# Optimization experiments

Measured on AMD Instinct MI355X. Metric: run time of the kernel, lower is better.

## Reference

```python
import jax, jax.numpy as jnp
import numpy as np

# RRFU config (matches init_kwargs)
S = 2          # scale_factor
G = 4          # groups
K = 3          # sample_k
C = 64         # in_channels
B, H, W_IN = 4, 128, 128
SC = S * S     # s_c
KC = K * K     # sample_c (3x3 = 9)


def setup_inputs() -> dict:
    key = jax.random.key(0)
    ks = jax.random.split(key, 9)
    x = jax.random.normal(ks[0], (B, C, H, W_IN), jnp.float32)
    # 1x1 conv weights stored as (out_ch, in_ch); std chosen per module's init
    # (mask convs are zero-init in the original; use small random so math is nontrivial)
    w_off = jax.random.normal(ks[1], (G * SC * 2, C), jnp.float32) * 0.001
    b_off = jnp.zeros((G * SC * 2,), jnp.float32)
    w_offm = jax.random.normal(ks[2], (G * SC * 2, C), jnp.float32) * 0.01
    b_offm = jnp.zeros((G * SC * 2,), jnp.float32)
    w_sk = jax.random.normal(ks[3], (KC, C), jnp.float32) * 0.005
    b_sk = jnp.zeros((KC,), jnp.float32)
    w_km = jax.random.normal(ks[4], (KC, C), jnp.float32) * 0.01
    b_km = jnp.zeros((KC,), jnp.float32)
    return {"x": x, "w_off": w_off, "b_off": b_off, "w_offm": w_offm,
            "b_offm": b_offm, "w_sk": w_sk, "b_sk": b_sk, "w_km": w_km, "b_km": b_km}


def _conv1x1(x, w, b):
    return jnp.einsum('oc,bchw->bohw', w, x) + b[None, :, None, None]


def _bilinear_border(img, iy, ix):
    """img: (Cg,H,W); iy,ix: (Ho,Wo) pixel coords. grid_sample bilinear, padding_mode='border'."""
    Hh, Ww = img.shape[1], img.shape[2]
    ix = jnp.clip(ix, 0.0, Ww - 1.0)
    iy = jnp.clip(iy, 0.0, Hh - 1.0)
    x0 = jnp.floor(ix)
    y0 = jnp.floor(iy)
    wx = ix - x0
    wy = iy - y0
    x0i = x0.astype(jnp.int32)
    y0i = y0.astype(jnp.int32)
    x1i = jnp.minimum(x0i + 1, Ww - 1)
    y1i = jnp.minimum(y0i + 1, Hh - 1)
    v00 = img[:, y0i, x0i]
    v01 = img[:, y0i, x1i]
    v10 = img[:, y1i, x0i]
    v11 = img[:, y1i, x1i]
    return (v00 * (1 - wx) * (1 - wy) + v01 * wx * (1 - wy)
            + v10 * (1 - wx) * wy + v11 * wx * wy)


def reference(x, w_off, b_off, w_offm, b_offm, w_sk, b_sk, w_km, b_km):
    b0, c0, h0, w0 = x.shape
    # learned offsets, gated by sigmoid mask
    off = _conv1x1(x, w_off, b_off) * jax.nn.sigmoid(_conv1x1(x, w_offm, b_offm))
    bg = b0 * G
    # (b, g*S*S*2, h, w) -> (bg, S, S, 2, h, w) -> (bg, h, S, w, S, 2) -> (bg, S*h, S*w, 2)
    off = off.reshape(bg, S, S, 2, h0, w0).transpose(0, 4, 1, 5, 2, 3).reshape(bg, S * h0, S * w0, 2)
    Ho, Wo = S * h0, S * w0
    # coord_base + offset, normalized then un-normalized for align_corners=False grid_sample
    cx = jnp.arange(Wo, dtype=x.dtype) + 0.5
    cy = jnp.arange(Ho, dtype=x.dtype) + 0.5
    ix = (cx[None, None, :] + off[..., 0]) * (w0 / Wo) - 0.5  # (bg, Ho, Wo)
    iy = (cy[None, :, None] + off[..., 1]) * (h0 / Ho) - 0.5
    x_r = x.reshape(bg, c0 // G, h0, w0)
    x_def = jax.vmap(_bilinear_border)(x_r, iy, ix).reshape(b0, c0, Ho, Wo)
    # CARAFE-style dynamic reassembly: softmax kernel over 3x3 neighborhood
    sk = _conv1x1(x_def, w_sk, b_sk) * jax.nn.sigmoid(_conv1x1(x_def, w_km, b_km))
    skn = jax.nn.softmax(sk, axis=1)  # (b, 9, Ho, Wo)
    pad = K // 2
    xp = jnp.pad(x_def, ((0, 0), (0, 0), (pad, pad), (pad, pad)))  # zero pad like F.unfold
    out = jnp.zeros_like(x_def)
    for ky in range(K):  # fixed 3x3 taps; avoids materializing (b,c,9,Ho,Wo)
        for kx in range(K):
            out = out + skn[:, ky * K + kx][:, None] * xp[:, :, ky:ky + Ho, kx:kx + Wo]
    return out
```

## Files before the change

### kernel.cpp

```cpp
#include <hip/hip_runtime.h>
#include <hip/hip_fp16.h>

constexpr int Bc  = 4;
constexpr int Cc  = 64;
constexpr int H0  = 128;
constexpr int W0  = 128;
constexpr int HW  = H0 * W0;
constexpr int Gc  = 4;
constexpr int CG  = Cc / Gc;
constexpr int HOc = H0 * 2;
constexpr int WOc = W0 * 2;

constexpr int TW = 16;
constexpr int TH = 8;
constexpr int HX = TW + 2;
constexpr int HY = TH + 2;
constexpr int NHALO = HX * HY;
constexpr int NTASK = Gc * NHALO;

constexpr int SXC = 10;
constexpr int SYC = 6;
constexpr int SN  = SXC * SYC;

__global__ __launch_bounds__(256) void k0_offsets(
    const float* __restrict__ x,
    const float* __restrict__ w_off,  const float* __restrict__ b_off,
    const float* __restrict__ w_offm, const float* __restrict__ b_offm,
    float* __restrict__ offbuf)
{
    const int bg = blockIdx.y;
    const int b  = bg >> 2, g = bg & 3;
    const int pp = blockIdx.x * 256 + threadIdx.x;
    const int h  = pp >> 6;
    const int w  = (pp & 63) << 1;

    const float2* xp = reinterpret_cast<const float2*>(
        x + (size_t)b * Cc * HW + h * W0 + w);
    const float* Wa = w_off  + (g * 8) * Cc;
    const float* Wm = w_offm + (g * 8) * Cc;

    float a0[8], a1[8], m0[8], m1[8];
#pragma unroll
    for (int r = 0; r < 8; ++r) { a0[r] = a1[r] = m0[r] = m1[r] = 0.f; }

#pragma unroll 4
    for (int c = 0; c < Cc; ++c) {
        const float2 xv = xp[c * (HW >> 1)];
#pragma unroll
        for (int r = 0; r < 8; ++r) {
            const float wa = Wa[r * Cc + c];
            const float wm = Wm[r * Cc + c];
            a0[r] = fmaf(wa, xv.x, a0[r]);
            a1[r] = fmaf(wa, xv.y, a1[r]);
            m0[r] = fmaf(wm, xv.x, m0[r]);
            m1[r] = fmaf(wm, xv.y, m1[r]);
        }
    }

    float* ob = offbuf + ((size_t)bg * 8) * HW + h * W0 + w;
#pragma unroll
    for (int r = 0; r < 8; ++r) {
        const float ba = b_off [g * 8 + r];
        const float bm = b_offm[g * 8 + r];
        const float o0 = (a0[r] + ba) / (1.f + __expf(-(m0[r] + bm)));
        const float o1 = (a1[r] + ba) / (1.f + __expf(-(m1[r] + bm)));
        *reinterpret_cast<float2*>(&ob[(size_t)r * HW]) = make_float2(o0, o1);
    }
}

__global__ __launch_bounds__(256) void k1_fused(
    const float* __restrict__ x, const float* __restrict__ offbuf,
    const float* __restrict__ w_sk, const float* __restrict__ b_sk,
    const float* __restrict__ w_km, const float* __restrict__ b_km,
    float* __restrict__ out)
{
    __shared__ __half xd[Cc][NHALO];
    __shared__ float  ovl[Cc * SN];
    float* xstage = ovl;
    float* kmb    = ovl;
    float* sknb   = ovl + 128 * 9;

    const int b    = blockIdx.y;
    const int tile = blockIdx.x;
    const int ox = (tile & 15) * TW;
    const int oy = (tile >> 4) * TH;
    const int t  = threadIdx.x;
    const int syr = (oy >> 1) - 1;
    const int sxr = (ox >> 1) - 1;

    const float* xb = x + (size_t)b * Cc * HW;

    for (int i = t; i < Cc * SN; i += 256) {
        const int c   = i / SN;
        const int rem = i - c * SN;
        const int r   = rem / SXC;
        const int j   = rem - r * SXC;
        const int yy  = min(max(syr + r, 0), H0 - 1);
        const int xx  = min(max(sxr + j, 0), W0 - 1);
        xstage[i] = xb[(size_t)c * HW + yy * W0 + xx];
    }
    __syncthreads();

    for (int task = t; task < NTASK; task += 256) {
        const int g   = task / NHALO;
        const int pix = task - g * NHALO;
        const int hy  = pix / HX;
        const int hx  = pix - hy * HX;
        const int gy  = oy - 1 + hy;
        const int gx  = ox - 1 + hx;
        if (gy < 0 || gy >= HOc || gx < 0 || gx >= WOc) {
#pragma unroll 4
            for (int c = 0; c < CG; ++c) xd[g * CG + c][pix] = __half(0.f);
            continue;
        }
        const int sy = gy & 1, sx = gx & 1;
        const int h  = gy >> 1, w  = gx >> 1;
        const int r0 = sy * 4 + sx * 2;
        const int bg = b * 4 + g;
        const size_t obase = ((size_t)bg * 8 + r0) * HW + h * W0 + w;
        const float offx = offbuf[obase];
        const float offy = offbuf[obase + HW];

        float ix = ((float)gx + 0.5f + offx) * 0.5f - 0.5f;
        float iy = ((float)gy + 0.5f + offy) * 0.5f - 0.5f;
        ix = fminf(fmaxf(ix, 0.f), (float)(W0 - 1));
        iy = fminf(fmaxf(iy, 0.f), (float)(H0 - 1));
        const float x0f = floorf(ix), y0f = floorf(iy);
        const float wx = ix - x0f,   wy = iy - y0f;
        const int x0 = (int)x0f, y0 = (int)y0f;
        const int x1 = min(x0 + 1, W0 - 1), y1 = min(y0 + 1, H0 - 1);
        const float w00 = (1.f - wx) * (1.f - wy);
        const float w01 = wx * (1.f - wy);
        const float w10 = (1.f - wx) * wy;
        const float w11 = wx * wy;

        const int j0 = x0 - sxr, j1 = x1 - sxr;
        const int i0 = y0 - syr, i1 = y1 - syr;
        const bool inl = (j0 >= 0) & (j1 < SXC) & (i0 >= 0) & (i1 < SYC);

        if (inl) {
            const int o00 = i0 * SXC + j0, o01 = i0 * SXC + j1;
            const int o10 = i1 * SXC + j0, o11 = i1 * SXC + j1;
            const float* s = xstage + (g * CG) * SN;
#pragma unroll 4
            for (int c = 0; c < CG; ++c) {
                const float* pc = s + c * SN;
                const float v = w00 * pc[o00] + w01 * pc[o01]
                              + w10 * pc[o10] + w11 * pc[o11];
                xd[g * CG + c][pix] = __float2half(v);
            }
        } else {
            const int o00 = y0 * W0 + x0, o01 = y0 * W0 + x1;
            const int o10 = y1 * W0 + x0, o11 = y1 * W0 + x1;
            const float* xg = xb + (size_t)(g * CG) * HW;
#pragma unroll 4
            for (int c = 0; c < CG; ++c) {
                const float* pc = xg + (size_t)c * HW;
                const float v = w00 * pc[o00] + w01 * pc[o01]
                              + w10 * pc[o10] + w11 * pc[o11];
                xd[g * CG + c][pix] = __float2half(v);
            }
        }
    }
    __syncthreads();

    {
        const int p   = t & 127;
        const int ctr = ((p >> 4) + 1) * HX + (p & 15) + 1;
        float acc[9];
#pragma unroll
        for (int k = 0; k < 9; ++k) acc[k] = 0.f;

        if (t < 128) {
            for (int c = 0; c < Cc; ++c) {
                const float xv = __half2float(xd[c][ctr]);
#pragma unroll
                for (int k = 0; k < 9; ++k)
                    acc[k] = fmaf(w_sk[k * Cc + c], xv, acc[k]);
            }
        } else {
            for (int c = 0; c < Cc; ++c) {
                const float xv = __half2float(xd[c][ctr]);
#pragma unroll
                for (int k = 0; k < 9; ++k)
                    acc[k] = fmaf(w_km[k * Cc + c], xv, acc[k]);
            }
#pragma unroll
            for (int k = 0; k < 9; ++k) kmb[p * 9 + k] = acc[k];
        }
        __syncthreads();

        if (t < 128) {
            float sv[9], mx = -1e30f;
#pragma unroll
            for (int k = 0; k < 9; ++k) {
                const float z = kmb[p * 9 + k] + b_km[k];
                sv[k] = (acc[k] + b_sk[k]) / (1.f + __expf(-z));
                mx = fmaxf(mx, sv[k]);
            }
            float sum = 0.f;
#pragma unroll
            for (int k = 0; k < 9; ++k) { sv[k] = __expf(sv[k] - mx); sum += sv[k]; }
            const float inv = 1.f / sum;
#pragma unroll
            for (int k = 0; k < 9; ++k) sknb[p * 9 + k] = sv[k] * inv;
        }
    }
    __syncthreads();

    {
        const int sq    = t & 31;
        const int chunk = t >> 5;
        const int sqx = sq & 7, sqy = sq >> 3;
        const int hx0 = 2 * sqx, hy0 = 2 * sqy;
        const int p00 = (2 * sqy) * TW + 2 * sqx;

        float s00[9], s01[9], s10[9], s11[9];
#pragma unroll
        for (int k = 0; k < 9; ++k) {
            s00[k] = sknb[p00 * 9 + k];        s01[k] = sknb[(p00 + 1) * 9 + k];
            s10[k] = sknb[(p00 + TW) * 9 + k]; s11[k] = sknb[(p00 + TW + 1) * 9 + k];
        }
        const int orow0 = oy + 2 * sqy, ocol0 = ox + 2 * sqx;

#pragma unroll 2
        for (int i = 0; i < 8; ++i) {
            const int c = chunk * 8 + i;
            const __half* xc = &xd[c][0];
            float wd[4][4];
#pragma unroll
            for (int ry = 0; ry < 4; ++ry) {
                const int base = (hy0 + ry) * HX + hx0;
                const __half2 u0 = *reinterpret_cast<const __half2*>(&xc[base]);
                const __half2 u1 = *reinterpret_cast<const __half2*>(&xc[base + 2]);
                const float2 f0 = __half22float2(u0);
                const float2 f1 = __half22float2(u1);
                wd[ry][0] = f0.x; wd[ry][1] = f0.y; wd[ry][2] = f1.x; wd[ry][3] = f1.y;
            }
            float a00 = 0.f, a01 = 0.f, a10 = 0.f, a11 = 0.f;
#pragma unroll
            for (int ky = 0; ky < 3; ++ky)
#pragma unroll
                for (int kx = 0; kx < 3; ++kx) {
                    const int k = ky * 3 + kx;
                    a00 = fmaf(s00[k], wd[ky    ][kx    ], a00);
                    a01 = fmaf(s01[k], wd[ky    ][kx + 1], a01);
                    a10 = fmaf(s10[k], wd[ky + 1][kx    ], a10);
                    a11 = fmaf(s11[k], wd[ky + 1][kx + 1], a11);
                }
            float* ob = out + ((size_t)(b * Cc + c)) * (HOc * WOc)
                            + (size_t)orow0 * WOc + ocol0;
            *reinterpret_cast<float2*>(ob)       = make_float2(a00, a01);
            *reinterpret_cast<float2*>(ob + WOc) = make_float2(a10, a11);
        }
    }
}

extern "C" void kernel_launch(void* const* d_in, const int* in_sizes, int n_in,
                              void* d_out, int out_size, void* d_ws, size_t ws_size,
                              hipStream_t stream)
{
    const float* x      = (const float*)d_in[0];
    const float* w_off  = (const float*)d_in[1];
    const float* b_off  = (const float*)d_in[2];
    const float* w_offm = (const float*)d_in[3];
    const float* b_offm = (const float*)d_in[4];
    const float* w_sk   = (const float*)d_in[5];
    const float* b_sk   = (const float*)d_in[6];
    const float* w_km   = (const float*)d_in[7];
    const float* b_km   = (const float*)d_in[8];
    float* outp = (float*)d_out;

    const size_t off_bytes = (size_t)Bc * Gc * 8 * HW * sizeof(float);
    if (ws_size < off_bytes) return;
    float* offbuf = (float*)d_ws;

    dim3 blk(256);
    dim3 g0(HW / (2 * 256), Bc * Gc);
    hipLaunchKernelGGL(k0_offsets, g0, blk, 0, stream,
                       x, w_off, b_off, w_offm, b_offm, offbuf);

    dim3 g1(512, Bc);
    hipLaunchKernelGGL(k1_fused, g1, blk, 0, stream,
                       x, offbuf, w_sk, b_sk, w_km, b_km, outp);
}
```

Measured before the change: 68.31 us.

## Fuse offset conv into main kernel and stage input via direct global-to-LDS loads

Removes the separate offset kernel and its global offset buffer. Each block now computes the gated offset 1x1 conv for its 10x6 source patch from the staged input in shared memory, and reads offsets from LDS. The input staging uses global_load_lds, the launch becomes a 1D grid with a swizzled block-to-tile mapping, and launch bounds request 3 blocks per CU. This trades a kernel launch and the offset-buffer round trip for redundant offset compute on halo pixels, extra LDS, and a serial 64-channel loop per block in which only 60 of 64 lanes per wave are active.

Result: slower. 151.0 us (+121.1%).

```diff
diff --git a/kernel.cpp b/kernel.cpp
--- a/kernel.cpp
+++ b/kernel.cpp
@@ -21,67 +21,36 @@
 constexpr int SXC = 10;
 constexpr int SYC = 6;
 constexpr int SN  = SXC * SYC;
-
-__global__ __launch_bounds__(256) void k0_offsets(
+constexpr int NROW = Gc * 8;
+
+constexpr int NTILE = (HOc / TH) * (WOc / TW);
+constexpr int NB    = NTILE * Bc;
+
+__device__ __forceinline__ void gl_lds4(const float* g, float* l) {
+    __builtin_amdgcn_global_load_lds(
+        (const __attribute__((address_space(1))) void*)g,
+        (__attribute__((address_space(3)))       void*)l, 4, 0, 0);
+}
+
+__global__ __launch_bounds__(256, 3) void k1_fused(
     const float* __restrict__ x,
     const float* __restrict__ w_off,  const float* __restrict__ b_off,
     const float* __restrict__ w_offm, const float* __restrict__ b_offm,
-    float* __restrict__ offbuf)
-{
-    const int bg = blockIdx.y;
-    const int b  = bg >> 2, g = bg & 3;
-    const int pp = blockIdx.x * 256 + threadIdx.x;
-    const int h  = pp >> 6;
-    const int w  = (pp & 63) << 1;
-
-    const float2* xp = reinterpret_cast<const float2*>(
-        x + (size_t)b * Cc * HW + h * W0 + w);
-    const float* Wa = w_off  + (g * 8) * Cc;
-    const float* Wm = w_offm + (g * 8) * Cc;
-
-    float a0[8], a1[8], m0[8], m1[8];
-#pragma unroll
-    for (int r = 0; r < 8; ++r) { a0[r] = a1[r] = m0[r] = m1[r] = 0.f; }
-
-#pragma unroll 4
-    for (int c = 0; c < Cc; ++c) {
-        const float2 xv = xp[c * (HW >> 1)];
-#pragma unroll
-        for (int r = 0; r < 8; ++r) {
-            const float wa = Wa[r * Cc + c];
-            const float wm = Wm[r * Cc + c];
-            a0[r] = fmaf(wa, xv.x, a0[r]);
-            a1[r] = fmaf(wa, xv.y, a1[r]);
-            m0[r] = fmaf(wm, xv.x, m0[r]);
-            m1[r] = fmaf(wm, xv.y, m1[r]);
-        }
-    }
-
-    float* ob = offbuf + ((size_t)bg * 8) * HW + h * W0 + w;
-#pragma unroll
-    for (int r = 0; r < 8; ++r) {
-        const float ba = b_off [g * 8 + r];
-        const float bm = b_offm[g * 8 + r];
-        const float o0 = (a0[r] + ba) / (1.f + __expf(-(m0[r] + bm)));
-        const float o1 = (a1[r] + ba) / (1.f + __expf(-(m1[r] + bm)));
-        *reinterpret_cast<float2*>(&ob[(size_t)r * HW]) = make_float2(o0, o1);
-    }
-}
-
-__global__ __launch_bounds__(256) void k1_fused(
-    const float* __restrict__ x, const float* __restrict__ offbuf,
-    const float* __restrict__ w_sk, const float* __restrict__ b_sk,
-    const float* __restrict__ w_km, const float* __restrict__ b_km,
+    const float* __restrict__ w_sk,   const float* __restrict__ b_sk,
+    const float* __restrict__ w_km,   const float* __restrict__ b_km,
     float* __restrict__ out)
 {
     __shared__ __half xd[Cc][NHALO];
+    __shared__ float  offs[NROW][SN];
     __shared__ float  ovl[Cc * SN];
     float* xstage = ovl;
     float* kmb    = ovl;
     float* sknb   = ovl + 128 * 9;
 
-    const int b    = blockIdx.y;
-    const int tile = blockIdx.x;
+    const int bid  = blockIdx.x;
+    const int sw   = (bid & 7) * (NB / 8) + (bid >> 3);
+    const int b    = sw >> 9;
+    const int tile = sw & 511;
     const int ox = (tile & 15) * TW;
     const int oy = (tile >> 4) * TH;
     const int t  = threadIdx.x;
@@ -97,7 +66,32 @@
         const int j   = rem - r * SXC;
         const int yy  = min(max(syr + r, 0), H0 - 1);
         const int xx  = min(max(sxr + j, 0), W0 - 1);
-        xstage[i] = xb[(size_t)c * HW + yy * W0 + xx];
+        gl_lds4(xb + (size_t)c * HW + yy * W0 + xx, &xstage[i]);
+    }
+    __syncthreads();
+
+    {
+        const int wave = t >> 6, lane = t & 63;
+        if (lane < SN) {
+            const int R0 = wave * 8;
+            float a[8], m[8];
+#pragma unroll
+            for (int q = 0; q < 8; ++q) { a[q] = 0.f; m[q] = 0.f; }
+            for (int c = 0; c < Cc; ++c) {
+                const float xv = xstage[c * SN + lane];
+#pragma unroll
+                for (int q = 0; q < 8; ++q) {
+                    a[q] = fmaf(w_off [(R0 + q) * Cc + c], xv, a[q]);
+                    m[q] = fmaf(w_offm[(R0 + q) * Cc + c], xv, m[q]);
+                }
+            }
+#pragma unroll
+            for (int q = 0; q < 8; ++q) {
+                const float av = a[q] + b_off [R0 + q];
+                const float mv = m[q] + b_offm[R0 + q];
+                offs[R0 + q][lane] = av / (1.f + __expf(-mv));
+            }
+        }
     }
     __syncthreads();
 
@@ -116,10 +110,9 @@
         const int sy = gy & 1, sx = gx & 1;
         const int h  = gy >> 1, w  = gx >> 1;
         const int r0 = sy * 4 + sx * 2;
-        const int bg = b * 4 + g;
-        const size_t obase = ((size_t)bg * 8 + r0) * HW + h * W0 + w;
-        const float offx = offbuf[obase];
-        const float offy = offbuf[obase + HW];
+        const int pos = (h - syr) * SXC + (w - sxr);
+        const float offx = offs[g * 8 + r0    ][pos];
+        const float offy = offs[g * 8 + r0 + 1][pos];
 
         float ix = ((float)gx + 0.5f + offx) * 0.5f - 0.5f;
         float iy = ((float)gy + 0.5f + offy) * 0.5f - 0.5f;
@@ -271,16 +264,9 @@
     const float* b_km   = (const float*)d_in[8];
     float* outp = (float*)d_out;
 
-    const size_t off_bytes = (size_t)Bc * Gc * 8 * HW * sizeof(float);
-    if (ws_size < off_bytes) return;
-    float* offbuf = (float*)d_ws;
-
     dim3 blk(256);
-    dim3 g0(HW / (2 * 256), Bc * Gc);
-    hipLaunchKernelGGL(k0_offsets, g0, blk, 0, stream,
-                       x, w_off, b_off, w_offm, b_offm, offbuf);
-
-    dim3 g1(512, Bc);
+    dim3 g1(NB);
     hipLaunchKernelGGL(k1_fused, g1, blk, 0, stream,
-                       x, offbuf, w_sk, b_sk, w_km, b_km, outp);
+                       x, w_off, b_off, w_offm, b_offm,
+                       w_sk, b_sk, w_km, b_km, outp);
 }
```
